# Performance work log

Measured on AMD Instinct MI355X. Metric: run time of the kernel, lower is better.

The kernel has to match this reference:

```python
import jax, jax.numpy as jnp
import numpy as np

N_NODES = 50000


def gcn_conv(x, W, b, src, dst, n_nodes):
    # PyG GCNConv: h = W x; out = D^{-1/2} (A + I) D^{-1/2} h + b
    h = x @ W  # [N, out_dim]
    ones = jnp.ones(src.shape[0], dtype=x.dtype)
    # degree with self-loops, counted on destination nodes
    deg = jax.ops.segment_sum(ones, dst, num_segments=n_nodes) + 1.0
    dinv = jax.lax.rsqrt(deg)  # deg >= 1, always safe
    norm = dinv[src] * dinv[dst]  # [E]
    agg = jax.ops.segment_sum(h[src] * norm[:, None], dst, num_segments=n_nodes)
    agg = agg + h * (dinv * dinv)[:, None]  # self-loop contribution
    return agg + b


def setup_inputs() -> dict:
    key = jax.random.key(0)
    k1, k2, k3, k4 = jax.random.split(key, 4)
    input_dim, hidden_dim, output_dim = 512, 256, 64
    n_edges = 1_600_000
    x = jax.random.normal(k1, (N_NODES, input_dim), dtype=jnp.float32)
    edge_index = jax.random.randint(k2, (2, n_edges), 0, N_NODES, dtype=jnp.int32)
    W1 = jax.random.normal(k3, (input_dim, hidden_dim), dtype=jnp.float32) / np.sqrt(input_dim)
    b1 = jnp.zeros((hidden_dim,), dtype=jnp.float32)
    W2 = jax.random.normal(k4, (hidden_dim, output_dim), dtype=jnp.float32) / np.sqrt(hidden_dim)
    b2 = jnp.zeros((output_dim,), dtype=jnp.float32)
    return {"x": x, "W1": W1, "b1": b1, "W2": W2, "b2": b2, "edge_index": edge_index}


def reference(x, W1, b1, W2, b2, edge_index):
    src, dst = edge_index[0], edge_index[1]
    h = jax.nn.relu(gcn_conv(x, W1, b1, src, dst, N_NODES))
    h = gcn_conv(h, W2, b2, src, dst, N_NODES)
    return jax.nn.log_softmax(h, axis=1)
```

## Files before the change

kernel.cpp:

```cpp
#include <hip/hip_runtime.h>

#define NODES 50000
#define NBIN 196
#define EPB 4096

typedef __attribute__((ext_vector_type(8))) short short8;
typedef __attribute__((ext_vector_type(4))) float f32x4;
typedef __attribute__((ext_vector_type(2))) float f32x2;

__device__ __forceinline__ ushort f2bf(float f) {
    uint u = __float_as_uint(f);
    uint r = (u + 0x7fffu + ((u >> 16) & 1u)) >> 16;
    return (ushort)r;
}
__device__ __forceinline__ float bf2f(ushort u) {
    return __uint_as_float(((uint)u) << 16);
}
__device__ __forceinline__ uchar f2fp8(float f) {
    return (uchar)(__builtin_amdgcn_cvt_pk_fp8_f32(f, f, 0, false) & 0xff);
}
__device__ __forceinline__ uint cvtpk_bf16(float lo, float hi) {
    uint r;
    asm("v_cvt_pk_bf16_f32 %0, %1, %2" : "=v"(r) : "v"(lo), "v"(hi));
    return r;
}


__global__ __launch_bounds__(256) void k_hist(const int* __restrict__ dst, int E,
                                              int* __restrict__ hist, int nblk) {
    __shared__ int h[NBIN];
    int t = threadIdx.x;
    for (int i = t; i < NBIN; i += 256) h[i] = 0;
    __syncthreads();
    int base = blockIdx.x * EPB;
#pragma unroll
    for (int i = 0; i < EPB / 256; ++i) {
        int e = base + i * 256 + t;
        if (e < E) atomicAdd(&h[dst[e] >> 8], 1);
    }
    __syncthreads();
    for (int i = t; i < NBIN; i += 256) hist[i * nblk + blockIdx.x] = h[i];
}

__global__ __launch_bounds__(1024) void k_scanbin(const int* __restrict__ hist,
                                                  int* __restrict__ offl,
                                                  int* __restrict__ btot, int nblk) {
    __shared__ int s[1024];
    int b = blockIdx.x, t = threadIdx.x;
    int v = (t < nblk) ? hist[b * nblk + t] : 0;
    s[t] = v;
    __syncthreads();
    for (int off = 1; off < 1024; off <<= 1) {
        int u = (t >= off) ? s[t - off] : 0;
        __syncthreads();
        s[t] += u;
        __syncthreads();
    }
    if (t < nblk) offl[b * nblk + t] = s[t] - v;
    if (t == 1023) btot[b] = s[1023];
}

__global__ __launch_bounds__(256) void k_scanoff(const int* __restrict__ btot,
                                                 int* __restrict__ binoff,
                                                 int* __restrict__ rowstart, int E) {
    __shared__ int s[256];
    int t = threadIdx.x;
    int v = (t < NBIN) ? btot[t] : 0;
    s[t] = v;
    __syncthreads();
    for (int off = 1; off < 256; off <<= 1) {
        int u = (t >= off) ? s[t - off] : 0;
        __syncthreads();
        s[t] += u;
        __syncthreads();
    }
    if (t < NBIN) binoff[t] = s[t] - v;
    if (t == 0) { binoff[NBIN] = E; rowstart[NODES] = E; }
}

__global__ __launch_bounds__(256) void k_part(const int* __restrict__ src,
                                              const int* __restrict__ dst, int E,
                                              const int* __restrict__ offl,
                                              const int* __restrict__ binoff, int nblk,
                                              uint* __restrict__ tmp) {
    __shared__ int cur[NBIN];
    int t = threadIdx.x, blk = blockIdx.x;
    for (int i = t; i < NBIN; i += 256) cur[i] = binoff[i] + offl[i * nblk + blk];
    __syncthreads();
    int base = blk * EPB;
#pragma unroll
    for (int i = 0; i < EPB / 256; ++i) {
        int e = base + i * 256 + t;
        if (e < E) {
            int d = dst[e];
            int p = atomicAdd(&cur[d >> 8], 1);
            tmp[p] = (uint)src[e] | ((uint)(d & 0xff) << 16);
        }
    }
}

__global__ __launch_bounds__(256) void k_csr(const uint* __restrict__ tmp,
                                             const int* __restrict__ binoff,
                                             int* __restrict__ rowstart,
                                             float* __restrict__ dinv,
                                             ushort* __restrict__ esrc16) {
    __shared__ int ncnt[256], nst[256];
    int b = blockIdx.x, t = threadIdx.x;
    int e0 = binoff[b], e1 = binoff[b + 1];
    int nb0 = b << 8;
    int nn = min(256, NODES - nb0);
    ncnt[t] = 0;
    __syncthreads();
    for (int e = e0 + t; e < e1; e += 256) atomicAdd(&ncnt[(tmp[e] >> 16) & 0xff], 1);
    __syncthreads();
    int v = ncnt[t];
    nst[t] = v;
    __syncthreads();
    for (int off = 1; off < 256; off <<= 1) {
        int u = (t >= off) ? nst[t - off] : 0;
        __syncthreads();
        nst[t] += u;
        __syncthreads();
    }
    int excl = nst[t] - v;
    if (t < nn) {
        rowstart[nb0 + t] = e0 + excl;
        dinv[nb0 + t] = rsqrtf(1.0f + (float)v);
    }
    __syncthreads();
    ncnt[t] = e0 + excl;
    __syncthreads();
    for (int e = e0 + t; e < e1; e += 256) {
        uint q = tmp[e];
        int p = atomicAdd(&ncnt[(q >> 16) & 0xff], 1);
        esrc16[p] = (ushort)(q & 0xffff);
    }
}

__global__ void k_wfill(const ushort* __restrict__ esrc16, const float* __restrict__ dinv,
                        uint* __restrict__ epack, int E) {
    int e4 = (blockIdx.x * blockDim.x + threadIdx.x) * 4;
    if (e4 + 3 < E) {
        ushort4 s = *(const ushort4*)(esrc16 + e4);
        uint4 o;
        o.x = (uint)s.x | ((uint)f2bf(dinv[s.x]) << 16);
        o.y = (uint)s.y | ((uint)f2bf(dinv[s.y]) << 16);
        o.z = (uint)s.z | ((uint)f2bf(dinv[s.z]) << 16);
        o.w = (uint)s.w | ((uint)f2bf(dinv[s.w]) << 16);
        *(uint4*)(epack + e4) = o;
    } else {
        for (int e = e4; e < E; ++e) {
            int s = esrc16[e];
            epack[e] = (uint)s | ((uint)f2bf(dinv[s]) << 16);
        }
    }
}

__global__ void k_cast2(const float* __restrict__ W1, ushort* __restrict__ w1t,
                        const float* __restrict__ W2, ushort* __restrict__ w2t) {
    const int N1 = 512 * 256;
    int i = blockIdx.x * blockDim.x + threadIdx.x;
    if (i < N1) {
        int r = i / 256, c = i % 256;
        w1t[(size_t)c * 512 + r] = f2bf(W1[i]);
    } else {
        int j = i - N1;
        if (j < 256 * 64) {
            int r = j / 64, c = j % 64;
            w2t[(size_t)c * 256 + r] = f2bf(W2[j]);
        }
    }
}

__global__ __launch_bounds__(256) void k_gemm1(const float* __restrict__ x,
                                               const ushort* __restrict__ w1t,
                                               uchar* __restrict__ h1f8, int M, int K) {
    constexpr int BM = 64, BN = 128, BK = 64;
    constexpr int NIT = 8;
    __shared__ __align__(16) ushort As[BM * BK];
    __shared__ __align__(16) ushort Bs[BN * BK];

    int t = threadIdx.x;
    int w = t >> 6, l = t & 63;
    int wm = w & 1, wn = w >> 1;
    int bm = (blockIdx.x >> 1) * BM;
    int bn = (blockIdx.x & 1) * BN;
    int lr = l & 15, g4 = l >> 4;

    f32x4 acc[2][4] = {};

    int ar = t >> 2;
    int aq = t & 3;
    int arow_g = bm + ar;
    bool aok = arow_g < M;
    const float* ap = x + (size_t)arow_g * K + aq * 16;
    char* adst = (char*)As + ar * 128;
    int aswz = (ar & 7) << 4;

    int brow_loc = l >> 3;
    int bseg = ((l & 7) << 4) ^ (brow_loc << 4);

    float4 fa[4];
    auto loadA = [&](int k0) {
#pragma unroll
        for (int j = 0; j < 4; ++j)
            fa[j] = aok ? *(const float4*)(ap + k0 + j * 4) : make_float4(0.f, 0.f, 0.f, 0.f);
    };
    auto writeA = [&]() {
#pragma unroll
        for (int j = 0; j < 2; ++j) {
            uint p0 = cvtpk_bf16(fa[2 * j].x, fa[2 * j].y);
            uint p1 = cvtpk_bf16(fa[2 * j].z, fa[2 * j].w);
            uint p2 = cvtpk_bf16(fa[2 * j + 1].x, fa[2 * j + 1].y);
            uint p3 = cvtpk_bf16(fa[2 * j + 1].z, fa[2 * j + 1].w);
            int4 v = make_int4((int)p0, (int)p1, (int)p2, (int)p3);
            *(int4*)(adst + ((aq * 32 + j * 16) ^ aswz)) = v;
        }
    };
    auto stageB = [&](int k0) {
#pragma unroll
        for (int i = 0; i < 4; ++i) {
            int rbase = w * 32 + i * 8;
            const char* gsrc = (const char*)w1t + (size_t)(bn + rbase + brow_loc) * (K * 2) + k0 * 2 + bseg;
            __builtin_amdgcn_global_load_lds(
                (const __attribute__((address_space(1))) uint*)gsrc,
                (__attribute__((address_space(3))) uint*)((char*)Bs + rbase * 128),
                16, 0, 0);
        }
    };
    auto compute = [&]() {
#pragma unroll
        for (int ks = 0; ks < 2; ++ks) {
            short8 af[2], bfr[4];
#pragma unroll
            for (int mt = 0; mt < 2; ++mt) {
                int r = wm * 32 + mt * 16 + lr;
                af[mt] = *(const short8*)((const char*)As + r * 128 + ((ks * 64 + g4 * 16) ^ ((r & 7) << 4)));
            }
#pragma unroll
            for (int nt = 0; nt < 4; ++nt) {
                int r = wn * 64 + nt * 16 + lr;
                bfr[nt] = *(const short8*)((const char*)Bs + r * 128 + ((ks * 64 + g4 * 16) ^ ((r & 7) << 4)));
            }
#pragma unroll
            for (int mt = 0; mt < 2; ++mt)
#pragma unroll
                for (int nt = 0; nt < 4; ++nt)
                    acc[mt][nt] = __builtin_amdgcn_mfma_f32_16x16x32_bf16(af[mt], bfr[nt], acc[mt][nt], 0, 0, 0);
        }
    };

    loadA(0);
    stageB(0);
    writeA();
    __syncthreads();

    for (int it = 0; it < NIT; ++it) {
        if (it + 1 < NIT) loadA((it + 1) * BK);
        compute();
        if (it + 1 < NIT) {
            __syncthreads();
            stageB((it + 1) * BK);
            writeA();
            __syncthreads();
        }
    }

#pragma unroll
    for (int mt = 0; mt < 2; ++mt)
#pragma unroll
        for (int nt = 0; nt < 4; ++nt)
#pragma unroll
            for (int i = 0; i < 4; ++i) {
                int row = bm + wm * 32 + mt * 16 + g4 * 4 + i;
                int col = bn + wn * 64 + nt * 16 + lr;
                if (row < M) h1f8[(size_t)row * 256 + col] = f2fp8(acc[mt][nt][i]);
            }
}

__global__ __launch_bounds__(256) void k_gemm2(const ushort* __restrict__ A,
                                               const ushort* __restrict__ Bt,
                                               ushort* __restrict__ Cb,
                                               int M, int K) {
    constexpr int BM = 64, BN = 64;
    constexpr int NT = 4;
    constexpr int SA = 40;
    __shared__ ushort As[BM * SA];
    __shared__ ushort Bs[BN * SA];

    int t = threadIdx.x;
    int w = t >> 6, l = t & 63;
    int bm = blockIdx.x * BM;
    int lr = l & 15, lk = (l >> 4) * 8;

    f32x4 acc[NT] = {};
    const int ACH = BM * 4;
    const int BCH = BN * 4;

    for (int k0 = 0; k0 < K; k0 += 32) {
        for (int c = t; c < ACH + BCH; c += 256) {
            if (c < ACH) {
                int row = c >> 2, seg = c & 3;
                int gr = bm + row;
                int4 v = make_int4(0, 0, 0, 0);
                if (gr < M) v = *(const int4*)(A + (size_t)gr * K + k0 + seg * 8);
                *(int4*)(&As[row * SA + seg * 8]) = v;
            } else {
                int cc = c - ACH;
                int row = cc >> 2, seg = cc & 3;
                int4 v = *(const int4*)(Bt + (size_t)row * K + k0 + seg * 8);
                *(int4*)(&Bs[row * SA + seg * 8]) = v;
            }
        }
        __syncthreads();
        short8 af = *(const short8*)(&As[(w * 16 + lr) * SA + lk]);
        short8 bfr[NT];
#pragma unroll
        for (int nt = 0; nt < NT; ++nt)
            bfr[nt] = *(const short8*)(&Bs[(nt * 16 + lr) * SA + lk]);
#pragma unroll
        for (int nt = 0; nt < NT; ++nt)
            acc[nt] = __builtin_amdgcn_mfma_f32_16x16x32_bf16(af, bfr[nt], acc[nt], 0, 0, 0);
        __syncthreads();
    }

#pragma unroll
    for (int nt = 0; nt < NT; ++nt)
#pragma unroll
        for (int i = 0; i < 4; ++i) {
            int row = bm + w * 16 + (l >> 4) * 4 + i;
            int col = nt * 16 + lr;
            if (row < M) Cb[(size_t)row * BN + col] = f2bf(acc[nt][i]);
        }
}

__global__ __launch_bounds__(256) void k_agg1(const uchar* __restrict__ h8,
                                              const int* __restrict__ rowstart,
                                              const uint* __restrict__ ep,
                                              const float* __restrict__ dinv,
                                              const float* __restrict__ b1,
                                              ushort* __restrict__ out) {
    int wave = __builtin_amdgcn_readfirstlane(threadIdx.x >> 6);
    int lane = threadIdx.x & 63;
    int n = blockIdx.x * 4 + wave;
    if (n >= NODES) return;
    const uchar* hl = h8 + lane * 4;
    float4 acc = make_float4(0.f, 0.f, 0.f, 0.f);
    int e0 = __builtin_amdgcn_readfirstlane(rowstart[n]);
    int e1 = __builtin_amdgcn_readfirstlane(rowstart[n + 1]);
    int e = e0;
#define A1_STEP(q, qv)                                                        \
    {                                                                         \
        float wt = __uint_as_float((q) & 0xffff0000u);                        \
        f32x2 lo = __builtin_amdgcn_cvt_pk_f32_fp8((int)(qv), false);         \
        f32x2 hi = __builtin_amdgcn_cvt_pk_f32_fp8((int)(qv), true);          \
        acc.x = fmaf(wt, lo[0], acc.x);                                       \
        acc.y = fmaf(wt, lo[1], acc.y);                                       \
        acc.z = fmaf(wt, hi[0], acc.z);                                       \
        acc.w = fmaf(wt, hi[1], acc.w);                                       \
    }
    for (; e + 8 <= e1; e += 8) {
        uint q0 = ep[e],     q1 = ep[e + 1], q2 = ep[e + 2], q3 = ep[e + 3];
        uint q4 = ep[e + 4], q5 = ep[e + 5], q6 = ep[e + 6], q7 = ep[e + 7];
        uint v0 = *(const uint*)(hl + (size_t)(q0 & 0xffff) * 256);
        uint v1 = *(const uint*)(hl + (size_t)(q1 & 0xffff) * 256);
        uint v2 = *(const uint*)(hl + (size_t)(q2 & 0xffff) * 256);
        uint v3 = *(const uint*)(hl + (size_t)(q3 & 0xffff) * 256);
        uint v4 = *(const uint*)(hl + (size_t)(q4 & 0xffff) * 256);
        uint v5 = *(const uint*)(hl + (size_t)(q5 & 0xffff) * 256);
        uint v6 = *(const uint*)(hl + (size_t)(q6 & 0xffff) * 256);
        uint v7 = *(const uint*)(hl + (size_t)(q7 & 0xffff) * 256);
        A1_STEP(q0, v0) A1_STEP(q1, v1) A1_STEP(q2, v2) A1_STEP(q3, v3)
        A1_STEP(q4, v4) A1_STEP(q5, v5) A1_STEP(q6, v6) A1_STEP(q7, v7)
    }
    for (; e < e1; ++e) {
        uint q = ep[e];
        uint v = *(const uint*)(hl + (size_t)(q & 0xffff) * 256);
        A1_STEP(q, v)
    }
#undef A1_STEP
    float dn = dinv[n];
    float s2v = dn * dn;
    uint qs = *(const uint*)(hl + (size_t)n * 256);
    f32x2 slo = __builtin_amdgcn_cvt_pk_f32_fp8((int)qs, false);
    f32x2 shi = __builtin_amdgcn_cvt_pk_f32_fp8((int)qs, true);
    float4 bb = *(const float4*)(b1 + lane * 4);
    ushort4 r;
    r.x = f2bf(fmaxf(fmaf(acc.x, dn, fmaf(slo[0], s2v, bb.x)), 0.f));
    r.y = f2bf(fmaxf(fmaf(acc.y, dn, fmaf(slo[1], s2v, bb.y)), 0.f));
    r.z = f2bf(fmaxf(fmaf(acc.z, dn, fmaf(shi[0], s2v, bb.z)), 0.f));
    r.w = f2bf(fmaxf(fmaf(acc.w, dn, fmaf(shi[1], s2v, bb.w)), 0.f));
    *(ushort4*)(out + (size_t)n * 256 + lane * 4) = r;
}

__global__ __launch_bounds__(256) void k_agg2(const ushort* __restrict__ h,
                                              const int* __restrict__ rowstart,
                                              const uint* __restrict__ ep,
                                              const float* __restrict__ dinv,
                                              const float* __restrict__ b2,
                                              float* __restrict__ out) {
    int wave = __builtin_amdgcn_readfirstlane(threadIdx.x >> 6);
    int lane = threadIdx.x & 63;
    int n = blockIdx.x * 4 + wave;
    if (n >= NODES) return;
    const ushort* hl = h + lane;
    float acc = 0.f;
    int e0 = __builtin_amdgcn_readfirstlane(rowstart[n]);
    int e1 = __builtin_amdgcn_readfirstlane(rowstart[n + 1]);
    int e = e0;
    for (; e + 8 <= e1; e += 8) {
        uint q0 = ep[e],     q1 = ep[e + 1], q2 = ep[e + 2], q3 = ep[e + 3];
        uint q4 = ep[e + 4], q5 = ep[e + 5], q6 = ep[e + 6], q7 = ep[e + 7];
        float v0 = bf2f(hl[(size_t)(q0 & 0xffff) * 64]);
        float v1 = bf2f(hl[(size_t)(q1 & 0xffff) * 64]);
        float v2 = bf2f(hl[(size_t)(q2 & 0xffff) * 64]);
        float v3 = bf2f(hl[(size_t)(q3 & 0xffff) * 64]);
        float v4 = bf2f(hl[(size_t)(q4 & 0xffff) * 64]);
        float v5 = bf2f(hl[(size_t)(q5 & 0xffff) * 64]);
        float v6 = bf2f(hl[(size_t)(q6 & 0xffff) * 64]);
        float v7 = bf2f(hl[(size_t)(q7 & 0xffff) * 64]);
        acc = fmaf(__uint_as_float(q0 & 0xffff0000u), v0, acc);
        acc = fmaf(__uint_as_float(q1 & 0xffff0000u), v1, acc);
        acc = fmaf(__uint_as_float(q2 & 0xffff0000u), v2, acc);
        acc = fmaf(__uint_as_float(q3 & 0xffff0000u), v3, acc);
        acc = fmaf(__uint_as_float(q4 & 0xffff0000u), v4, acc);
        acc = fmaf(__uint_as_float(q5 & 0xffff0000u), v5, acc);
        acc = fmaf(__uint_as_float(q6 & 0xffff0000u), v6, acc);
        acc = fmaf(__uint_as_float(q7 & 0xffff0000u), v7, acc);
    }
    for (; e < e1; ++e) {
        uint q = ep[e];
        acc = fmaf(__uint_as_float(q & 0xffff0000u), bf2f(hl[(size_t)(q & 0xffff) * 64]), acc);
    }
    float dn = dinv[n];
    float r = fmaf(acc, dn, fmaf(bf2f(hl[(size_t)n * 64]), dn * dn, b2[lane]));
    float m = r;
#pragma unroll
    for (int off = 32; off; off >>= 1) m = fmaxf(m, __shfl_xor(m, off));
    float ex = __expf(r - m);
    float ssum = ex;
#pragma unroll
    for (int off = 32; off; off >>= 1) ssum += __shfl_xor(ssum, off);
    out[(size_t)n * 64 + lane] = r - m - __logf(ssum);
}


extern "C" void kernel_launch(void* const* d_in, const int* in_sizes, int n_in,
                              void* d_out, int out_size, void* d_ws, size_t ws_size,
                              hipStream_t stream) {
    const float* x  = (const float*)d_in[0];
    const float* W1 = (const float*)d_in[1];
    const float* b1 = (const float*)d_in[2];
    const float* W2 = (const float*)d_in[3];
    const float* b2 = (const float*)d_in[4];
    const int*   ei = (const int*)d_in[5];
    int E = in_sizes[5] / 2;
    const int* src = ei;
    const int* dst = ei + E;
    float* out = (float*)d_out;

    int nblk = (E + EPB - 1) / EPB;

    char* wsp = (char*)d_ws;
    auto alloc = [&](size_t bytes) {
        char* p = wsp;
        wsp += (bytes + 255) & ~(size_t)255;
        return p;
    };
    int*    hist     = (int*)alloc((size_t)NBIN * nblk * 4);
    int*    offl     = (int*)alloc((size_t)NBIN * nblk * 4);
    int*    btot     = (int*)alloc((size_t)NBIN * 4);
    int*    binoff   = (int*)alloc((size_t)(NBIN + 1) * 4);
    int*    rowstart = (int*)alloc((size_t)(NODES + 1) * 4);
    float*  dinv     = (float*)alloc((size_t)NODES * 4);
    uint*   tmp      = (uint*)alloc((size_t)E * 4);
    ushort* esrc16   = (ushort*)alloc((size_t)E * 2);
    uint*   epack    = (uint*)alloc((size_t)E * 4);
    ushort* w1t      = (ushort*)alloc((size_t)256 * 512 * 2);
    ushort* w2t      = (ushort*)alloc((size_t)64 * 256 * 2);
    uchar*  h1f8     = (uchar*)alloc((size_t)NODES * 256);
    ushort* h1ab     = (ushort*)alloc((size_t)NODES * 256 * 2);
    ushort* h2b      = (ushort*)alloc((size_t)NODES * 64 * 2);

    k_hist<<<nblk, 256, 0, stream>>>(dst, E, hist, nblk);
    k_scanbin<<<NBIN, 1024, 0, stream>>>(hist, offl, btot, nblk);
    k_scanoff<<<1, 256, 0, stream>>>(btot, binoff, rowstart, E);
    k_part<<<nblk, 256, 0, stream>>>(src, dst, E, offl, binoff, nblk, tmp);
    k_csr<<<NBIN, 256, 0, stream>>>(tmp, binoff, rowstart, dinv, esrc16);
    k_wfill<<<(E / 4 + 255) / 256, 256, 0, stream>>>(esrc16, dinv, epack, E);

    k_cast2<<<(512 * 256 + 256 * 64 + 255) / 256, 256, 0, stream>>>(W1, w1t, W2, w2t);

    k_gemm1<<<((NODES + 63) / 64) * 2, 256, 0, stream>>>(x, w1t, h1f8, NODES, 512);
    k_agg1<<<(NODES + 3) / 4, 256, 0, stream>>>(h1f8, rowstart, epack, dinv, b1, h1ab);

    k_gemm2<<<(NODES + 63) / 64, 256, 0, stream>>>(h1ab, w2t, h2b, NODES, 256);
    k_agg2<<<(NODES + 3) / 4, 256, 0, stream>>>(h2b, rowstart, epack, dinv, b2, out);
}
```

Baseline: 199.0 us.

## Fuse layer-1 aggregation with layer-2 GEMM through shared memory

Merges the first aggregation kernel and the second GEMM into one kernel. Each block aggregates 16 nodes, writes their bf16 rows into an XOR-swizzled shared-memory tile, then runs MFMA against W2 to produce h2 directly. This removes the round trip of the 50000x256 bf16 intermediate through global memory and one kernel launch. In exchange, each wave now aggregates four nodes in sequence, which cuts parallelism per block. W2 is also reread from global or L2 memory by every block.

```diff
diff --git a/kernel.cpp b/kernel.cpp
--- a/kernel.cpp
+++ b/kernel.cpp
@@ -278,119 +278,89 @@
             }
 }
 
-__global__ __launch_bounds__(256) void k_gemm2(const ushort* __restrict__ A,
-                                               const ushort* __restrict__ Bt,
-                                               ushort* __restrict__ Cb,
-                                               int M, int K) {
-    constexpr int BM = 64, BN = 64;
-    constexpr int NT = 4;
-    constexpr int SA = 40;
-    __shared__ ushort As[BM * SA];
-    __shared__ ushort Bs[BN * SA];
-
+__global__ __launch_bounds__(256) void k_agg1g2(const uchar* __restrict__ h8,
+                                                const int* __restrict__ rowstart,
+                                                const uint* __restrict__ ep,
+                                                const float* __restrict__ dinv,
+                                                const float* __restrict__ b1,
+                                                const ushort* __restrict__ w2t,
+                                                ushort* __restrict__ h2b) {
+    __shared__ __align__(16) ushort rows[16 * 256];
     int t = threadIdx.x;
-    int w = t >> 6, l = t & 63;
-    int bm = blockIdx.x * BM;
-    int lr = l & 15, lk = (l >> 4) * 8;
-
-    f32x4 acc[NT] = {};
-    const int ACH = BM * 4;
-    const int BCH = BN * 4;
-
-    for (int k0 = 0; k0 < K; k0 += 32) {
-        for (int c = t; c < ACH + BCH; c += 256) {
-            if (c < ACH) {
-                int row = c >> 2, seg = c & 3;
-                int gr = bm + row;
-                int4 v = make_int4(0, 0, 0, 0);
-                if (gr < M) v = *(const int4*)(A + (size_t)gr * K + k0 + seg * 8);
-                *(int4*)(&As[row * SA + seg * 8]) = v;
-            } else {
-                int cc = c - ACH;
-                int row = cc >> 2, seg = cc & 3;
-                int4 v = *(const int4*)(Bt + (size_t)row * K + k0 + seg * 8);
-                *(int4*)(&Bs[row * SA + seg * 8]) = v;
-            }
-        }
-        __syncthreads();
-        short8 af = *(const short8*)(&As[(w * 16 + lr) * SA + lk]);
-        short8 bfr[NT];
-#pragma unroll
-        for (int nt = 0; nt < NT; ++nt)
-            bfr[nt] = *(const short8*)(&Bs[(nt * 16 + lr) * SA + lk]);
-#pragma unroll
-        for (int nt = 0; nt < NT; ++nt)
-            acc[nt] = __builtin_amdgcn_mfma_f32_16x16x32_bf16(af, bfr[nt], acc[nt], 0, 0, 0);
-        __syncthreads();
-    }
-
-#pragma unroll
-    for (int nt = 0; nt < NT; ++nt)
-#pragma unroll
-        for (int i = 0; i < 4; ++i) {
-            int row = bm + w * 16 + (l >> 4) * 4 + i;
-            int col = nt * 16 + lr;
-            if (row < M) Cb[(size_t)row * BN + col] = f2bf(acc[nt][i]);
-        }
-}
-
-__global__ __launch_bounds__(256) void k_agg1(const uchar* __restrict__ h8,
-                                              const int* __restrict__ rowstart,
-                                              const uint* __restrict__ ep,
-                                              const float* __restrict__ dinv,
-                                              const float* __restrict__ b1,
-                                              ushort* __restrict__ out) {
-    int wave = __builtin_amdgcn_readfirstlane(threadIdx.x >> 6);
-    int lane = threadIdx.x & 63;
-    int n = blockIdx.x * 4 + wave;
-    if (n >= NODES) return;
+    int w = __builtin_amdgcn_readfirstlane(t >> 6);
+    int lane = t & 63;
+    int nb = blockIdx.x * 16;
     const uchar* hl = h8 + lane * 4;
-    float4 acc = make_float4(0.f, 0.f, 0.f, 0.f);
-    int e0 = __builtin_amdgcn_readfirstlane(rowstart[n]);
-    int e1 = __builtin_amdgcn_readfirstlane(rowstart[n + 1]);
-    int e = e0;
+
+    for (int i = 0; i < 4; ++i) {
+        int r = w * 4 + i;
+        int n = nb + r;
+        float4 acc = make_float4(0.f, 0.f, 0.f, 0.f);
+        int e0 = __builtin_amdgcn_readfirstlane(rowstart[n]);
+        int e1 = __builtin_amdgcn_readfirstlane(rowstart[n + 1]);
+        int e = e0;
 #define A1_STEP(q, qv)                                                        \
-    {                                                                         \
-        float wt = __uint_as_float((q) & 0xffff0000u);                        \
-        f32x2 lo = __builtin_amdgcn_cvt_pk_f32_fp8((int)(qv), false);         \
-        f32x2 hi = __builtin_amdgcn_cvt_pk_f32_fp8((int)(qv), true);          \
-        acc.x = fmaf(wt, lo[0], acc.x);                                       \
-        acc.y = fmaf(wt, lo[1], acc.y);                                       \
-        acc.z = fmaf(wt, hi[0], acc.z);                                       \
-        acc.w = fmaf(wt, hi[1], acc.w);                                       \
-    }
-    for (; e + 8 <= e1; e += 8) {
-        uint q0 = ep[e],     q1 = ep[e + 1], q2 = ep[e + 2], q3 = ep[e + 3];
-        uint q4 = ep[e + 4], q5 = ep[e + 5], q6 = ep[e + 6], q7 = ep[e + 7];
-        uint v0 = *(const uint*)(hl + (size_t)(q0 & 0xffff) * 256);
-        uint v1 = *(const uint*)(hl + (size_t)(q1 & 0xffff) * 256);
-        uint v2 = *(const uint*)(hl + (size_t)(q2 & 0xffff) * 256);
-        uint v3 = *(const uint*)(hl + (size_t)(q3 & 0xffff) * 256);
-        uint v4 = *(const uint*)(hl + (size_t)(q4 & 0xffff) * 256);
-        uint v5 = *(const uint*)(hl + (size_t)(q5 & 0xffff) * 256);
-        uint v6 = *(const uint*)(hl + (size_t)(q6 & 0xffff) * 256);
-        uint v7 = *(const uint*)(hl + (size_t)(q7 & 0xffff) * 256);
-        A1_STEP(q0, v0) A1_STEP(q1, v1) A1_STEP(q2, v2) A1_STEP(q3, v3)
-        A1_STEP(q4, v4) A1_STEP(q5, v5) A1_STEP(q6, v6) A1_STEP(q7, v7)
-    }
-    for (; e < e1; ++e) {
-        uint q = ep[e];
-        uint v = *(const uint*)(hl + (size_t)(q & 0xffff) * 256);
-        A1_STEP(q, v)
-    }
+        {                                                                     \
+            float wt = __uint_as_float((q) & 0xffff0000u);                    \
+            f32x2 lo = __builtin_amdgcn_cvt_pk_f32_fp8((int)(qv), false);     \
+            f32x2 hi = __builtin_amdgcn_cvt_pk_f32_fp8((int)(qv), true);      \
+            acc.x = fmaf(wt, lo[0], acc.x);                                   \
+            acc.y = fmaf(wt, lo[1], acc.y);                                   \
+            acc.z = fmaf(wt, hi[0], acc.z);                                   \
+            acc.w = fmaf(wt, hi[1], acc.w);                                   \
+        }
+        for (; e + 8 <= e1; e += 8) {
+            uint q0 = ep[e],     q1 = ep[e + 1], q2 = ep[e + 2], q3 = ep[e + 3];
+            uint q4 = ep[e + 4], q5 = ep[e + 5], q6 = ep[e + 6], q7 = ep[e + 7];
+            uint v0 = *(const uint*)(hl + (size_t)(q0 & 0xffff) * 256);
+            uint v1 = *(const uint*)(hl + (size_t)(q1 & 0xffff) * 256);
+            uint v2 = *(const uint*)(hl + (size_t)(q2 & 0xffff) * 256);
+            uint v3 = *(const uint*)(hl + (size_t)(q3 & 0xffff) * 256);
+            uint v4 = *(const uint*)(hl + (size_t)(q4 & 0xffff) * 256);
+            uint v5 = *(const uint*)(hl + (size_t)(q5 & 0xffff) * 256);
+            uint v6 = *(const uint*)(hl + (size_t)(q6 & 0xffff) * 256);
+            uint v7 = *(const uint*)(hl + (size_t)(q7 & 0xffff) * 256);
+            A1_STEP(q0, v0) A1_STEP(q1, v1) A1_STEP(q2, v2) A1_STEP(q3, v3)
+            A1_STEP(q4, v4) A1_STEP(q5, v5) A1_STEP(q6, v6) A1_STEP(q7, v7)
+        }
+        for (; e < e1; ++e) {
+            uint q = ep[e];
+            uint v = *(const uint*)(hl + (size_t)(q & 0xffff) * 256);
+            A1_STEP(q, v)
+        }
 #undef A1_STEP
-    float dn = dinv[n];
-    float s2v = dn * dn;
-    uint qs = *(const uint*)(hl + (size_t)n * 256);
-    f32x2 slo = __builtin_amdgcn_cvt_pk_f32_fp8((int)qs, false);
-    f32x2 shi = __builtin_amdgcn_cvt_pk_f32_fp8((int)qs, true);
-    float4 bb = *(const float4*)(b1 + lane * 4);
-    ushort4 r;
-    r.x = f2bf(fmaxf(fmaf(acc.x, dn, fmaf(slo[0], s2v, bb.x)), 0.f));
-    r.y = f2bf(fmaxf(fmaf(acc.y, dn, fmaf(slo[1], s2v, bb.y)), 0.f));
-    r.z = f2bf(fmaxf(fmaf(acc.z, dn, fmaf(shi[0], s2v, bb.z)), 0.f));
-    r.w = f2bf(fmaxf(fmaf(acc.w, dn, fmaf(shi[1], s2v, bb.w)), 0.f));
-    *(ushort4*)(out + (size_t)n * 256 + lane * 4) = r;
+        float dn = dinv[n];
+        float s2v = dn * dn;
+        uint qs = *(const uint*)(hl + (size_t)n * 256);
+        f32x2 slo = __builtin_amdgcn_cvt_pk_f32_fp8((int)qs, false);
+        f32x2 shi = __builtin_amdgcn_cvt_pk_f32_fp8((int)qs, true);
+        float4 bb = *(const float4*)(b1 + lane * 4);
+        float rx = fmaxf(fmaf(acc.x, dn, fmaf(slo[0], s2v, bb.x)), 0.f);
+        float ry = fmaxf(fmaf(acc.y, dn, fmaf(slo[1], s2v, bb.y)), 0.f);
+        float rz = fmaxf(fmaf(acc.z, dn, fmaf(shi[0], s2v, bb.z)), 0.f);
+        float rw = fmaxf(fmaf(acc.w, dn, fmaf(shi[1], s2v, bb.w)), 0.f);
+        uint p0 = cvtpk_bf16(rx, ry);
+        uint p1 = cvtpk_bf16(rz, rw);
+        *(uint2*)((char*)rows + r * 512 + ((lane * 8) ^ ((r & 7) << 4))) =
+            make_uint2(p0, p1);
+    }
+    __syncthreads();
+
+    int lr = lane & 15, g4 = lane >> 4;
+    f32x4 acc2 = {};
+    const ushort* bcol = w2t + (size_t)(w * 16 + lr) * 256;
+#pragma unroll
+    for (int ks = 0; ks < 8; ++ks) {
+        short8 af = *(const short8*)((const char*)rows + lr * 512 +
+                                     ((ks * 64 + g4 * 16) ^ ((lr & 7) << 4)));
+        short8 bf = *(const short8*)(bcol + ks * 32 + g4 * 8);
+        acc2 = __builtin_amdgcn_mfma_f32_16x16x32_bf16(af, bf, acc2, 0, 0, 0);
+    }
+#pragma unroll
+    for (int i = 0; i < 4; ++i) {
+        int node = nb + g4 * 4 + i;
+        h2b[(size_t)node * 64 + w * 16 + lr] = f2bf(acc2[i]);
+    }
 }
 
 __global__ __launch_bounds__(256) void k_agg2(const ushort* __restrict__ h,
@@ -479,7 +449,6 @@
     ushort* w1t      = (ushort*)alloc((size_t)256 * 512 * 2);
     ushort* w2t      = (ushort*)alloc((size_t)64 * 256 * 2);
     uchar*  h1f8     = (uchar*)alloc((size_t)NODES * 256);
-    ushort* h1ab     = (ushort*)alloc((size_t)NODES * 256 * 2);
     ushort* h2b      = (ushort*)alloc((size_t)NODES * 64 * 2);
 
     k_hist<<<nblk, 256, 0, stream>>>(dst, E, hist, nblk);
@@ -492,8 +461,8 @@
     k_cast2<<<(512 * 256 + 256 * 64 + 255) / 256, 256, 0, stream>>>(W1, w1t, W2, w2t);
 
     k_gemm1<<<((NODES + 63) / 64) * 2, 256, 0, stream>>>(x, w1t, h1f8, NODES, 512);
-    k_agg1<<<(NODES + 3) / 4, 256, 0, stream>>>(h1f8, rowstart, epack, dinv, b1, h1ab);
-
-    k_gemm2<<<(NODES + 63) / 64, 256, 0, stream>>>(h1ab, w2t, h2b, NODES, 256);
+
+    k_agg1g2<<<NODES / 16, 256, 0, stream>>>(h1f8, rowstart, epack, dinv, b1, w2t, h2b);
+
     k_agg2<<<(NODES + 3) / 4, 256, 0, stream>>>(h2b, rowstart, epack, dinv, b2, out);
 }
```

New measurement: 197.0 us (median of 2 runs). No clear change (-1.0%).
